# Kernel tuning notes

Hardware: AMD Instinct MI355X
Metric: run time of the kernel (lower is better)

Reference implementation:

```python
import jax, jax.numpy as jnp
import numpy as np

# Matcher hyperparameters (from __init__ defaults)
COST_CLASS = 1.0
COST_CENTER = 5.0
COST_IOU = 2.0
CENTER_THRESHOLD = 2.0
INF_REPLACE = 1000000.0

B, Q, N, NUM_CLASSES = 64, 4096, 256, 20
SCENE_EXTENT = 50.0  # meters; box centers uniform in [0, 50]


def setup_inputs() -> dict:
    key = jax.random.key(0)
    k1, k2, k3, k4, k5, k6 = jax.random.split(key, 6)
    pred_logits = jax.random.normal(k1, (B, Q, NUM_CLASSES + 1), dtype=jnp.float32)
    pred_centers = jax.random.uniform(k2, (B, Q, 3), dtype=jnp.float32) * SCENE_EXTENT
    pred_sizes = jax.random.uniform(k3, (B, Q, 3), dtype=jnp.float32) * 2.5 + 0.5
    pred_boxes = jnp.concatenate([pred_centers, pred_sizes], axis=-1)  # [B,Q,6]
    tgt_centers = jax.random.uniform(k4, (B, N, 3), dtype=jnp.float32) * SCENE_EXTENT
    tgt_sizes = jax.random.uniform(k5, (B, N, 3), dtype=jnp.float32) * 2.5 + 0.5
    target_boxes = jnp.concatenate([tgt_centers, tgt_sizes], axis=-1)  # [B,N,6]
    target_labels = jax.random.randint(k6, (B, N), 0, NUM_CLASSES)  # all valid fg classes
    return {
        "pred_logits": pred_logits,
        "pred_boxes": pred_boxes,
        "target_labels": target_labels,
        "target_boxes": target_boxes,
    }


def _pairwise_iou3d(pred_boxes, target_boxes):
    # pred_boxes [B,Q,6], target_boxes [B,N,6] -> iou [B,Q,N]
    c1, s1 = pred_boxes[..., :3], pred_boxes[..., 3:]
    c2, s2 = target_boxes[..., :3], target_boxes[..., 3:]
    min1 = (c1 - s1 * 0.5)[:, :, None, :]  # [B,Q,1,3]
    max1 = (c1 + s1 * 0.5)[:, :, None, :]
    min2 = (c2 - s2 * 0.5)[:, None, :, :]  # [B,1,N,3]
    max2 = (c2 + s2 * 0.5)[:, None, :, :]
    inter_size = jnp.clip(jnp.minimum(max1, max2) - jnp.maximum(min1, min2), 0.0)
    inter_vol = jnp.prod(inter_size, axis=-1)  # [B,Q,N]
    vol1 = jnp.prod(s1, axis=-1)[:, :, None]  # [B,Q,1]
    vol2 = jnp.prod(s2, axis=-1)[:, None, :]  # [B,1,N]
    union = vol1 + vol2 - inter_vol
    return jnp.where(union > 0, inter_vol / union, 0.0)


def reference(pred_logits, pred_boxes, target_labels, target_boxes):
    # Class cost: -softmax prob of the target's class (foreground classes only)
    probs_fg = jax.nn.softmax(pred_logits, axis=-1)[..., :-1]  # [B,Q,C]
    class_cost = -jax.vmap(lambda p, l: p[:, l])(probs_fg, target_labels)  # [B,Q,N]

    # Center distance cost with threshold gating (torch.cdist = euclidean)
    pc = pred_boxes[..., :3]
    tc = target_boxes[..., :3]
    dist = jnp.sqrt(jnp.sum((pc[:, :, None, :] - tc[:, None, :, :]) ** 2, axis=-1))
    center_cost = jnp.where(dist <= CENTER_THRESHOLD, dist, jnp.inf)

    # 3D IoU cost
    iou_cost = 1.0 - _pairwise_iou3d(pred_boxes, target_boxes)

    total = COST_CLASS * class_cost + COST_CENTER * center_cost + COST_IOU * iou_cost
    total = jnp.where(jnp.isinf(total), INF_REPLACE, total)
    return total  # [B,Q,N] cost matrix fed to the (CPU) Hungarian solver
```

## Files before the change

### kernel.cpp

```cpp
#include <hip/hip_runtime.h>
#include <math.h>

#define BQ 64
#define QQ 4096
#define NN 256
#define NC 20
#define NL 21
#define TQ 256

__global__ __launch_bounds__(256)
void matcher_kernel(const float* __restrict__ logits,
                    const float* __restrict__ pboxes,
                    const int*   __restrict__ tlabels,
                    const float* __restrict__ tboxes,
                    float* __restrict__ out) {
    __shared__ float smq[TQ * 32];
    const int tid = threadIdx.x;
    const int b   = blockIdx.y;
    const int q0  = blockIdx.x * TQ;

    {
        const int q = q0 + tid;
        const float* lg = logits + (size_t)(b * QQ + q) * NL;
        float l[NL];
        #pragma unroll
        for (int c = 0; c < NL; ++c) l[c] = lg[c];
        float m = l[0];
        #pragma unroll
        for (int c = 1; c < NL; ++c) m = fmaxf(m, l[c]);
        float e[NL];
        float s = 0.f;
        #pragma unroll
        for (int c = 0; c < NL; ++c) { e[c] = expf(l[c] - m); s += e[c]; }
        const float rs = 1.0f / s;

        const float* pb = pboxes + (size_t)(b * QQ + q) * 6;
        float pcx = pb[0], pcy = pb[1], pcz = pb[2];
        float psx = pb[3], psy = pb[4], psz = pb[5];
        float* rec = smq + tid * 32;
        rec[0] = pcx; rec[1] = pcy; rec[2] = pcz;
        rec[3] = psx * psy * psz;
        rec[4] = pcx - psx * 0.5f; rec[5] = pcy - psy * 0.5f; rec[6] = pcz - psz * 0.5f;
        rec[7] = pcx + psx * 0.5f; rec[8] = pcy + psy * 0.5f; rec[9] = pcz + psz * 0.5f;
        #pragma unroll
        for (int c = 0; c < NC; ++c) rec[10 + c] = -(e[c] * rs);
    }

    const float* tb = tboxes + (size_t)(b * NN + tid) * 6;
    const float tcx = tb[0], tcy = tb[1], tcz = tb[2];
    const float tsx = tb[3], tsy = tb[4], tsz = tb[5];
    const float tminx = tcx - tsx * 0.5f, tminy = tcy - tsy * 0.5f, tminz = tcz - tsz * 0.5f;
    const float tmaxx = tcx + tsx * 0.5f, tmaxy = tcy + tsy * 0.5f, tmaxz = tcz + tsz * 0.5f;
    const float vol2  = tsx * tsy * tsz;
    const int   lab   = tlabels[b * NN + tid];

    __syncthreads();

    float* op = out + (size_t)(b * QQ + q0) * NN + tid;
    #pragma unroll 4
    for (int qq = 0; qq < TQ; ++qq) {
        const float* rec = smq + qq * 32;
        const float pcx = rec[0], pcy = rec[1], pcz = rec[2], vol1 = rec[3];
        const float mnx = rec[4], mny = rec[5], mnz = rec[6];
        const float mxx = rec[7], mxy = rec[8], mxz = rec[9];
        const float negp = rec[10 + lab];

        const float dx = __fsub_rn(pcx, tcx);
        const float dy = __fsub_rn(pcy, tcy);
        const float dz = __fsub_rn(pcz, tcz);
        const float d2 = __fadd_rn(__fadd_rn(__fmul_rn(dx, dx), __fmul_rn(dy, dy)),
                                   __fmul_rn(dz, dz));
        const float dist = __fsqrt_rn(d2);

        const float ix = fmaxf(fminf(mxx, tmaxx) - fmaxf(mnx, tminx), 0.f);
        const float iy = fmaxf(fminf(mxy, tmaxy) - fmaxf(mny, tminy), 0.f);
        const float iz = fmaxf(fminf(mxz, tmaxz) - fmaxf(mnz, tminz), 0.f);
        const float iv  = ix * iy * iz;
        const float uni = vol1 + vol2 - iv;
        const float iou = iv * __frcp_rn(uni);

        const float t = negp + 5.0f * dist + 2.0f - 2.0f * iou;
        const float r = (dist <= 2.0f) ? t : 1000000.0f;

        op[(size_t)qq * NN] = r;
    }
}

extern "C" void kernel_launch(void* const* d_in, const int* in_sizes, int n_in,
                              void* d_out, int out_size, void* d_ws, size_t ws_size,
                              hipStream_t stream) {
    const float* logits = (const float*)d_in[0];
    const float* pboxes = (const float*)d_in[1];
    const int*   tlabels = (const int*)d_in[2];
    const float* tboxes = (const float*)d_in[3];
    float* out = (float*)d_out;

    dim3 grid(QQ / TQ, BQ);
    matcher_kernel<<<grid, dim3(256), 0, stream>>>(logits, pboxes, tlabels, tboxes, out);
}
```

Measured before the change: 341.3 us.

## Restructure matcher to 4 targets per thread with float4 stores and split LDS

Each thread now handles four consecutive targets and writes them with one float4 store, while each wave walks every fourth query. The shared query records are split into a 12-float geometry array read as float4 and a transposed, padded probability array indexed by label. The correctly rounded sqrt and reciprocal are replaced with the hardware approximate intrinsics, and the distance gate now tests squared distance against a threshold. These changes aim to cut LDS traffic, store instruction count and ALU cost per output, at the price of more registers per thread and small rounding differences from the approximate sqrt and reciprocal.

```diff
diff --git a/kernel.cpp b/kernel.cpp
--- a/kernel.cpp
+++ b/kernel.cpp
@@ -7,6 +7,10 @@
 #define NC 20
 #define NL 21
 #define TQ 256
+#define GEO_STRIDE 12
+#define PROB_STRIDE 257
+
+#define GATE_D2 0x1.000001p+2f
 
 __global__ __launch_bounds__(256)
 void matcher_kernel(const float* __restrict__ logits,
@@ -14,7 +18,8 @@
                     const int*   __restrict__ tlabels,
                     const float* __restrict__ tboxes,
                     float* __restrict__ out) {
-    __shared__ float smq[TQ * 32];
+    __shared__ __align__(16) float geo[TQ * GEO_STRIDE];
+    __shared__ float prob[NC * PROB_STRIDE];
     const int tid = threadIdx.x;
     const int b   = blockIdx.y;
     const int q0  = blockIdx.x * TQ;
@@ -33,66 +38,79 @@
         #pragma unroll
         for (int c = 0; c < NL; ++c) { e[c] = expf(l[c] - m); s += e[c]; }
         const float rs = 1.0f / s;
+        #pragma unroll
+        for (int c = 0; c < NC; ++c)
+            prob[c * PROB_STRIDE + tid] = -(e[c] * rs);
 
         const float* pb = pboxes + (size_t)(b * QQ + q) * 6;
-        float pcx = pb[0], pcy = pb[1], pcz = pb[2];
-        float psx = pb[3], psy = pb[4], psz = pb[5];
-        float* rec = smq + tid * 32;
-        rec[0] = pcx; rec[1] = pcy; rec[2] = pcz;
-        rec[3] = psx * psy * psz;
-        rec[4] = pcx - psx * 0.5f; rec[5] = pcy - psy * 0.5f; rec[6] = pcz - psz * 0.5f;
-        rec[7] = pcx + psx * 0.5f; rec[8] = pcy + psy * 0.5f; rec[9] = pcz + psz * 0.5f;
-        #pragma unroll
-        for (int c = 0; c < NC; ++c) rec[10 + c] = -(e[c] * rs);
+        const float pcx = pb[0], pcy = pb[1], pcz = pb[2];
+        const float psx = pb[3], psy = pb[4], psz = pb[5];
+        float4* gp = (float4*)(geo + tid * GEO_STRIDE);
+        gp[0] = make_float4(pcx, pcy, pcz, psx * psy * psz);
+        gp[1] = make_float4(pcx - psx * 0.5f, pcy - psy * 0.5f, pcz - psz * 0.5f, 0.f);
+        gp[2] = make_float4(pcx + psx * 0.5f, pcy + psy * 0.5f, pcz + psz * 0.5f, 0.f);
     }
 
-    const float* tb = tboxes + (size_t)(b * NN + tid) * 6;
-    const float tcx = tb[0], tcy = tb[1], tcz = tb[2];
-    const float tsx = tb[3], tsy = tb[4], tsz = tb[5];
-    const float tminx = tcx - tsx * 0.5f, tminy = tcy - tsy * 0.5f, tminz = tcz - tsz * 0.5f;
-    const float tmaxx = tcx + tsx * 0.5f, tmaxy = tcy + tsy * 0.5f, tmaxz = tcz + tsz * 0.5f;
-    const float vol2  = tsx * tsy * tsz;
-    const int   lab   = tlabels[b * NN + tid];
+    const int lane = tid & 63;
+    const int w    = tid >> 6;
+    const int n0   = lane * 4;
+    float tcx[4], tcy[4], tcz[4];
+    float mn_x[4], mn_y[4], mn_z[4], mx_x[4], mx_y[4], mx_z[4], v2[4];
+    int plab[4];
+    #pragma unroll
+    for (int j = 0; j < 4; ++j) {
+        const float* tb = tboxes + (size_t)(b * NN + n0 + j) * 6;
+        const float cx = tb[0], cy = tb[1], cz = tb[2];
+        const float sx = tb[3], sy = tb[4], sz = tb[5];
+        tcx[j] = cx; tcy[j] = cy; tcz[j] = cz;
+        mn_x[j] = cx - sx * 0.5f; mn_y[j] = cy - sy * 0.5f; mn_z[j] = cz - sz * 0.5f;
+        mx_x[j] = cx + sx * 0.5f; mx_y[j] = cy + sy * 0.5f; mx_z[j] = cz + sz * 0.5f;
+        v2[j]   = sx * sy * sz;
+        plab[j] = tlabels[b * NN + n0 + j] * PROB_STRIDE;
+    }
 
     __syncthreads();
 
-    float* op = out + (size_t)(b * QQ + q0) * NN + tid;
-    #pragma unroll 4
-    for (int qq = 0; qq < TQ; ++qq) {
-        const float* rec = smq + qq * 32;
-        const float pcx = rec[0], pcy = rec[1], pcz = rec[2], vol1 = rec[3];
-        const float mnx = rec[4], mny = rec[5], mnz = rec[6];
-        const float mxx = rec[7], mxy = rec[8], mxz = rec[9];
-        const float negp = rec[10 + lab];
+    float* ob = out + ((size_t)(b * QQ + q0)) * NN + n0;
+    #pragma unroll 2
+    for (int qq = w; qq < TQ; qq += 4) {
+        const float4* gp = (const float4*)(geo + qq * GEO_STRIDE);
+        const float4 g0 = gp[0];
+        const float4 g1 = gp[1];
+        const float4 g2 = gp[2];
+        float r[4];
+        #pragma unroll
+        for (int j = 0; j < 4; ++j) {
+            const float negp = prob[plab[j] + qq];
 
-        const float dx = __fsub_rn(pcx, tcx);
-        const float dy = __fsub_rn(pcy, tcy);
-        const float dz = __fsub_rn(pcz, tcz);
-        const float d2 = __fadd_rn(__fadd_rn(__fmul_rn(dx, dx), __fmul_rn(dy, dy)),
-                                   __fmul_rn(dz, dz));
-        const float dist = __fsqrt_rn(d2);
+            const float dx = __fsub_rn(g0.x, tcx[j]);
+            const float dy = __fsub_rn(g0.y, tcy[j]);
+            const float dz = __fsub_rn(g0.z, tcz[j]);
+            const float d2 = __fadd_rn(__fadd_rn(__fmul_rn(dx, dx), __fmul_rn(dy, dy)),
+                                       __fmul_rn(dz, dz));
+            const float dist = __builtin_amdgcn_sqrtf(d2);
 
-        const float ix = fmaxf(fminf(mxx, tmaxx) - fmaxf(mnx, tminx), 0.f);
-        const float iy = fmaxf(fminf(mxy, tmaxy) - fmaxf(mny, tminy), 0.f);
-        const float iz = fmaxf(fminf(mxz, tmaxz) - fmaxf(mnz, tminz), 0.f);
-        const float iv  = ix * iy * iz;
-        const float uni = vol1 + vol2 - iv;
-        const float iou = iv * __frcp_rn(uni);
+            const float ix = fmaxf(fminf(g2.x, mx_x[j]) - fmaxf(g1.x, mn_x[j]), 0.f);
+            const float iy = fmaxf(fminf(g2.y, mx_y[j]) - fmaxf(g1.y, mn_y[j]), 0.f);
+            const float iz = fmaxf(fminf(g2.z, mx_z[j]) - fmaxf(g1.z, mn_z[j]), 0.f);
+            const float iv  = ix * iy * iz;
+            const float uni = g0.w + v2[j] - iv;
+            const float iou = iv * __builtin_amdgcn_rcpf(uni);
 
-        const float t = negp + 5.0f * dist + 2.0f - 2.0f * iou;
-        const float r = (dist <= 2.0f) ? t : 1000000.0f;
-
-        op[(size_t)qq * NN] = r;
+            const float t = fmaf(5.0f, dist, negp) + fmaf(-2.0f, iou, 2.0f);
+            r[j] = (d2 <= GATE_D2) ? t : 1000000.0f;
+        }
+        *(float4*)(ob + (size_t)qq * NN) = make_float4(r[0], r[1], r[2], r[3]);
     }
 }
 
 extern "C" void kernel_launch(void* const* d_in, const int* in_sizes, int n_in,
                               void* d_out, int out_size, void* d_ws, size_t ws_size,
                               hipStream_t stream) {
-    const float* logits = (const float*)d_in[0];
-    const float* pboxes = (const float*)d_in[1];
+    const float* logits  = (const float*)d_in[0];
+    const float* pboxes  = (const float*)d_in[1];
     const int*   tlabels = (const int*)d_in[2];
-    const float* tboxes = (const float*)d_in[3];
+    const float* tboxes  = (const float*)d_in[3];
     float* out = (float*)d_out;
 
     dim3 grid(QQ / TQ, BQ);
```

New measurement: 302.8 us. 1.13x faster.
